# Performance work log

Hardware: AMD Instinct MI355X
Metric: run time of the kernel (lower is better)

## Reference

```python
import jax, jax.numpy as jnp
import numpy as np
import math

B, S, D = 4, 4096, 256

def _linear(x, W, b):
    return jnp.einsum('bsd,ed->bse', x, W) + b

def _attn(x, Wq, bq, Wk, bk, Wv, bv, d):
    Q = _linear(x, Wq, bq)
    K = _linear(x, Wk, bk)
    V = _linear(x, Wv, bv)
    scores = jnp.einsum('bqd,bkd->bqk', Q, K) / math.sqrt(d)  # [B,S,S]
    w = jax.nn.softmax(scores, axis=-1)
    return jnp.einsum('bqk,bkd->bqd', w, V)

def setup_inputs() -> dict:
    key = jax.random.key(0)
    ks = jax.random.split(key, 32)
    p = {}
    p['x'] = jax.random.normal(ks[0], (B, S, D), dtype=jnp.float32)
    p['eps'] = jax.random.normal(ks[1], (B, S, D), dtype=jnp.float32)
    i = 2
    for name in ['Wq1','Wk1','Wv1','Wq2','Wk2','Wv2','Wmu','Wlv']:
        p[name] = 0.02 * jax.random.normal(ks[i], (D, D), dtype=jnp.float32); i += 1
    for name in ['bq1','bk1','bv1','bq2','bk2','bv2','bmu','blv']:
        p[name] = jnp.zeros((D,), dtype=jnp.float32)
    p['Wg'] = 0.02 * jax.random.normal(ks[i], (1, D), dtype=jnp.float32); i += 1
    p['bg'] = jnp.zeros((1,), dtype=jnp.float32)
    p['gamma'] = jnp.ones((D,), dtype=jnp.float32)
    p['beta'] = jnp.zeros((D,), dtype=jnp.float32)
    return p

def reference(x, eps, Wq1, Wk1, Wv1, Wq2, Wk2, Wv2, Wmu, Wlv,
              bq1, bk1, bv1, bq2, bk2, bv2, bmu, blv, Wg, bg, gamma, beta):
    d = x.shape[-1]
    h1 = _attn(x, Wq1, bq1, Wk1, bk1, Wv1, bv1, d)
    h2 = _attn(h1, Wq2, bq2, Wk2, bk2, Wv2, bv2, d)
    mu = _linear(h2, Wmu, bmu)
    logvar = _linear(h2, Wlv, blv)
    std = jnp.exp(0.5 * logvar)
    z = jax.nn.elu(mu + eps * std)
    p_gate = jax.nn.sigmoid(_linear(h2.mean(axis=1)[:, None, :], Wg, bg))[:, 0, 0]  # [B]
    y = x + z
    mean = y.mean(axis=-1, keepdims=True)
    var = y.var(axis=-1, keepdims=True)
    out = (y - mean) / jnp.sqrt(var + 1e-5) * gamma + beta
    return (out, mu, logvar, p_gate)
```

## Files before the change

kernel.cpp:

```cpp
#include <hip/hip_runtime.h>
#include <hip/hip_bf16.h>
#include <hip/hip_fp8.h>
#include <cstdint>
#include <cstddef>


#define S_LEN 4096
#define DMODEL 256
#define NBATCH 4
#define MTOT (NBATCH * S_LEN)

typedef __bf16 bf16;
typedef __bf16 bf16x8 __attribute__((ext_vector_type(8)));
typedef float f32x4 __attribute__((ext_vector_type(4)));
typedef float f32x16 __attribute__((ext_vector_type(16)));
typedef unsigned char u8;
typedef unsigned int u32;

__device__ __forceinline__ f32x4 mfma16(bf16x8 a, bf16x8 b, f32x4 c) {
  return __builtin_amdgcn_mfma_f32_16x16x32_bf16(a, b, c, 0, 0, 0);
}
__device__ __forceinline__ f32x16 mfma32f8(long a, long b, f32x16 c) {
  return __builtin_amdgcn_mfma_f32_32x32x16_fp8_fp8(a, b, c, 0, 0, 0);
}

__device__ __forceinline__ void async16(const void* g, void* lds) {
  __builtin_amdgcn_global_load_lds(
      (const __attribute__((address_space(1))) unsigned int*)g,
      (__attribute__((address_space(3))) unsigned int*)lds, 16, 0, 0);
}

__device__ __forceinline__ unsigned short f2bfbits(float f) {
  return __builtin_bit_cast(unsigned short, (bf16)f);
}
__device__ __forceinline__ u8 f2fp8(float f) {
  __hip_fp8_e4m3 t(f);
  return *(u8*)&t;
}

struct WPtrs { const float* p[8]; };

__global__ void cast_all_kernel(const f32x4* __restrict__ x, WPtrs wp,
                                ushort4* __restrict__ x16, ushort4* __restrict__ w16) {
  int bx = blockIdx.x, t = threadIdx.x;
  const f32x4* src;
  ushort4* dst;
  if (bx < 4096) {
    src = x + (size_t)bx * 256 + t;
    dst = x16 + (size_t)bx * 256 + t;
  } else {
    int r = bx - 4096;
    int m = r >> 6;
    int i = (r & 63) * 256 + t;
    src = (const f32x4*)wp.p[m] + i;
    dst = w16 + (size_t)m * 16384 + i;
  }
  f32x4 v = *src;
  ushort4 o;
  o.x = f2bfbits(v[0]); o.y = f2bfbits(v[1]); o.z = f2bfbits(v[2]); o.w = f2bfbits(v[3]);
  *dst = o;
}

struct GemmIO {
  const float* bias[3];
  void* out[3];
};

__global__ __launch_bounds__(256, 3) void gemm_qkv_kernel(const bf16* __restrict__ A,
                                                          const bf16* __restrict__ Wb,
                                                          GemmIO io) {
  __shared__ bf16 ldsA[128 * 64];
  __shared__ bf16 ldsB[128 * 64];
  const int t = threadIdx.x;
  const int m0 = blockIdx.x * 128;
  const int n0 = blockIdx.y * 128;
  const bf16* W = Wb + (size_t)blockIdx.z * 65536;
  const int w = t >> 6, l = t & 63, lm = l & 15, q = l >> 4;
  const int wr = (w >> 1) * 64, wc = (w & 1) * 64;

  f32x4 acc[4][4] = {};
#pragma unroll 1
  for (int it = 0; it < 4; ++it) {
    const int k0 = it * 64;
#pragma unroll
    for (int c = 0; c < 4; ++c) {
      int i = c * 256 + t;
      int r = i >> 3, c8 = (i & 7) ^ (r & 7);
      async16(A + (size_t)(m0 + r) * 256 + k0 + c8 * 8, &ldsA[i * 8]);
    }
#pragma unroll
    for (int c = 0; c < 4; ++c) {
      int i = c * 256 + t;
      int r = i >> 3, c8 = (i & 7) ^ (r & 7);
      async16(W + (size_t)(n0 + r) * 256 + k0 + c8 * 8, &ldsB[i * 8]);
    }
    __syncthreads();
#pragma unroll
    for (int ks = 0; ks < 2; ++ks) {
      bf16x8 af[4], bfr[4];
#pragma unroll
      for (int i = 0; i < 4; ++i) {
        int ra = wr + i * 16 + lm;
        af[i] = *(const bf16x8*)&ldsA[ra * 64 + ((((ks << 2) + q) ^ (ra & 7)) << 3)];
        int rb = wc + i * 16 + lm;
        bfr[i] = *(const bf16x8*)&ldsB[rb * 64 + ((((ks << 2) + q) ^ (rb & 7)) << 3)];
      }
#pragma unroll
      for (int i = 0; i < 4; ++i)
#pragma unroll
        for (int jj = 0; jj < 4; ++jj) acc[i][jj] = mfma16(af[i], bfr[jj], acc[i][jj]);
    }
    __syncthreads();
  }
  const float* bias = io.bias[blockIdx.z];
  if (blockIdx.z == 2) {
    bf16* out = (bf16*)io.out[2];
#pragma unroll
    for (int jj = 0; jj < 4; ++jj) {
      int col = n0 + wc + jj * 16 + lm;
      float bv = bias[col];
#pragma unroll
      for (int i = 0; i < 4; ++i) {
        int row = m0 + wr + i * 16 + q * 4;
#pragma unroll
        for (int r = 0; r < 4; ++r)
          out[(size_t)(row + r) * 256 + col] = (bf16)(acc[i][jj][r] + bv);
      }
    }
  } else {
    u8* out = (u8*)io.out[blockIdx.z];
#pragma unroll
    for (int jj = 0; jj < 4; ++jj) {
      int col = n0 + wc + jj * 16 + lm;
      float bv = bias[col];
#pragma unroll
      for (int i = 0; i < 4; ++i) {
        int row = m0 + wr + i * 16 + q * 4;
#pragma unroll
        for (int r = 0; r < 4; ++r)
          out[(size_t)(row + r) * 256 + col] = f2fp8(acc[i][jj][r] + bv);
      }
    }
  }
}

__global__ __launch_bounds__(256, 3) void gemm_f_kernel(const bf16* __restrict__ A,
                                                        const bf16* __restrict__ Wb, GemmIO io) {
  __shared__ bf16 ldsA[128 * 64];
  __shared__ bf16 ldsB[128 * 64];
  const int t = threadIdx.x;
  const int m0 = blockIdx.x * 128;
  const int n0 = blockIdx.y * 128;
  const bf16* W = Wb + (size_t)blockIdx.z * 65536;
  const int w = t >> 6, l = t & 63, lm = l & 15, q = l >> 4;
  const int wr = (w >> 1) * 64, wc = (w & 1) * 64;

  f32x4 acc[4][4] = {};
#pragma unroll 1
  for (int it = 0; it < 4; ++it) {
    const int k0 = it * 64;
#pragma unroll
    for (int c = 0; c < 4; ++c) {
      int i = c * 256 + t;
      int r = i >> 3, c8 = (i & 7) ^ (r & 7);
      async16(A + (size_t)(m0 + r) * 256 + k0 + c8 * 8, &ldsA[i * 8]);
    }
#pragma unroll
    for (int c = 0; c < 4; ++c) {
      int i = c * 256 + t;
      int r = i >> 3, c8 = (i & 7) ^ (r & 7);
      async16(W + (size_t)(n0 + r) * 256 + k0 + c8 * 8, &ldsB[i * 8]);
    }
    __syncthreads();
#pragma unroll
    for (int ks = 0; ks < 2; ++ks) {
      bf16x8 af[4], bfr[4];
#pragma unroll
      for (int i = 0; i < 4; ++i) {
        int ra = wr + i * 16 + lm;
        af[i] = *(const bf16x8*)&ldsA[ra * 64 + ((((ks << 2) + q) ^ (ra & 7)) << 3)];
        int rb = wc + i * 16 + lm;
        bfr[i] = *(const bf16x8*)&ldsB[rb * 64 + ((((ks << 2) + q) ^ (rb & 7)) << 3)];
      }
#pragma unroll
      for (int i = 0; i < 4; ++i)
#pragma unroll
        for (int jj = 0; jj < 4; ++jj) acc[i][jj] = mfma16(af[i], bfr[jj], acc[i][jj]);
    }
    __syncthreads();
  }
  const float* bias = io.bias[blockIdx.z];
  float* out = (float*)io.out[blockIdx.z];
#pragma unroll
  for (int jj = 0; jj < 4; ++jj) {
    int col = n0 + wc + jj * 16 + lm;
    float bv = bias[col];
#pragma unroll
    for (int i = 0; i < 4; ++i) {
      int row = m0 + wr + i * 16 + q * 4;
#pragma unroll
      for (int r = 0; r < 4; ++r)
        out[(size_t)(row + r) * 256 + col] = acc[i][jj][r] + bv;
    }
  }
}

__global__ void transpose_kernel(const bf16* __restrict__ src, u8* __restrict__ dst) {
  __shared__ bf16 tile[64][72];
  int s0 = blockIdx.x * 64, d0 = blockIdx.y * 64;
  size_t boff = (size_t)blockIdx.z * S_LEN * 256;
  size_t boffT = (size_t)blockIdx.z * 256 * S_LEN;
  int t = threadIdx.x;
#pragma unroll
  for (int rep = 0; rep < 16; ++rep) {
    int lin = rep * 256 + t;
    int r = lin >> 6, c = lin & 63;
    tile[r][c] = src[boff + (size_t)(s0 + r) * 256 + d0 + c];
  }
  __syncthreads();
#pragma unroll
  for (int rep = 0; rep < 16; ++rep) {
    int lin = rep * 256 + t;
    int r = lin >> 6, c = lin & 63;
    dst[boffT + (size_t)(d0 + r) * S_LEN + s0 + c] = f2fp8((float)tile[c][r]);
  }
}

__global__ __launch_bounds__(1024, 4) void flash_kernel(const u8* __restrict__ Q,
                                                        const u8* __restrict__ K,
                                                        const u8* __restrict__ Vt,
                                                        bf16* __restrict__ O) {
  __shared__ __align__(16) u8 ldsK[256 * 256];
  __shared__ __align__(16) u8 ldsV[256 * 256];
  __shared__ __align__(16) u8 ldsP[2 * 32 * 264];
  __shared__ float lb[64];

  const int id = blockIdx.x;
  const int xcd = id & 7;
  const int b = xcd >> 1;
  const int qt = (id >> 3) + ((xcd & 1) << 5);

  const u8* Qb = Q + (size_t)b * S_LEN * 256;
  const u8* Kb = K + (size_t)b * S_LEN * 256;
  const u8* Vb = Vt + (size_t)b * 256 * S_LEN;
  bf16* Ob = O + (size_t)b * S_LEN * 256;

  const int t = threadIdx.x, w = t >> 6, lane = t & 63;
  const int m31 = lane & 31, kh = lane >> 5;
  const int qg = w & 1, sub = w >> 1;
  const float CL2 = 0.09016844005556021f;

  if (t < 64) lb[t] = 0.f;

  int sld[4], skg[4], svg[4];
#pragma unroll
  for (int it = 0; it < 4; ++it) {
    int c = it * 1024 + t;
    sld[it] = c * 16;
    int kr = c >> 4, g = (c & 15) ^ (kr & 15);
    skg[it] = kr * 256 + g * 16;
    svg[it] = kr * S_LEN + g * 16;
  }
  const int kn = sub * 32 + m31;
  const int kbase = kn * 256 + kh * 8, knx = kn & 15;
  const int vd = sub * 32 + m31;
  const int vbase = vd * 256 + kh * 8, vdx = vd & 15;
  u8* pstore = &ldsP[qg * 8448 + m31 * 264 + sub * 32 + 4 * kh];
  const u8* pread = &ldsP[qg * 8448 + m31 * 264 + kh * 8];

  long qf[16];
  {
    const u8* qrow = Qb + (size_t)(qt * 64 + qg * 32 + m31) * 256 + kh * 8;
#pragma unroll
    for (int ks = 0; ks < 16; ++ks) qf[ks] = *(const long*)(qrow + ks * 16);
  }

  f32x16 o_acc = {};
  float l_w = 0.f;

#pragma unroll
  for (int it = 0; it < 4; ++it) async16(Kb + skg[it], &ldsK[sld[it]]);

#pragma unroll 1
  for (int j = 0; j < 16; ++j) {
    __syncthreads();
    {
      const u8* vg = Vb + j * 256;
#pragma unroll
      for (int it = 0; it < 4; ++it) async16(vg + svg[it], &ldsV[sld[it]]);
    }
    f32x16 s = {};
#pragma unroll
    for (int ks = 0; ks < 16; ++ks) {
      long kf = *(const long*)(&ldsK[kbase + ((ks ^ knx) << 4)]);
      s = mfma32f8(kf, qf[ks], s);
    }
    float p[16];
#pragma unroll
    for (int r = 0; r < 16; ++r) {
      p[r] = __builtin_amdgcn_exp2f(s[r] * CL2);
      l_w += p[r];
    }
#pragma unroll
    for (int g = 0; g < 4; ++g) {
      u32 pk = (u32)f2fp8(p[4 * g]) | ((u32)f2fp8(p[4 * g + 1]) << 8) |
               ((u32)f2fp8(p[4 * g + 2]) << 16) | ((u32)f2fp8(p[4 * g + 3]) << 24);
      *(u32*)(pstore + g * 8) = pk;
    }
    __syncthreads();
    if (j + 1 < 16) {
      const u8* kg = Kb + (size_t)(j + 1) * 65536;
#pragma unroll
      for (int it = 0; it < 4; ++it) async16(kg + skg[it], &ldsK[sld[it]]);
    }
#pragma unroll
    for (int ks = 0; ks < 16; ++ks) {
      long pa = *(const long*)(pread + ks * 16);
      long vf = *(const long*)(&ldsV[vbase + ((ks ^ vdx) << 4)]);
      o_acc = mfma32f8(pa, vf, o_acc);
    }
  }

  l_w += __shfl_xor(l_w, 32, 64);
  if (kh == 0) atomicAdd(&lb[qg * 32 + m31], l_w);
  __syncthreads();

  bf16* orow = Ob + (size_t)(qt * 64 + qg * 32) * 256 + sub * 32;
#pragma unroll
  for (int reg = 0; reg < 16; ++reg) {
    const int row = (reg & 3) + 8 * (reg >> 2) + 4 * kh;
    orow[(size_t)row * 256 + m31] = (bf16)(o_acc[reg] / lb[qg * 32 + row]);
  }
}

__global__ __launch_bounds__(256) void gate_partial(const bf16* __restrict__ h,
                                                    float* __restrict__ part) {
  int bb = blockIdx.y;
  const bf16* hb = h + (size_t)bb * S_LEN * 256 + (size_t)blockIdx.x * 64 * 256;
  int t = threadIdx.x;
  float acc = 0.f;
#pragma unroll 4
  for (int s = 0; s < 64; ++s) acc += (float)hb[s * 256 + t];
  part[((size_t)bb * 64 + blockIdx.x) * 256 + t] = acc;
}

__global__ __launch_bounds__(256) void gate_final(const float* __restrict__ part,
                                                  const float* __restrict__ Wg,
                                                  const float* __restrict__ bg,
                                                  float* __restrict__ pg) {
  int bb = blockIdx.x, t = threadIdx.x;
  const float* p = part + (size_t)bb * 64 * 256;
  float acc = 0.f;
#pragma unroll 4
  for (int c = 0; c < 64; ++c) acc += p[c * 256 + t];
  acc *= Wg[t] * (1.0f / 4096.0f);
  __shared__ float red[256];
  red[t] = acc;
  __syncthreads();
  if (t < 64) {
    float a = red[t] + red[t + 64] + red[t + 128] + red[t + 192];
#pragma unroll
    for (int d = 1; d < 64; d <<= 1) a += __shfl_xor(a, d, 64);
    if (t == 0) pg[bb] = 1.0f / (1.0f + __expf(-(a + bg[0])));
  }
}

__global__ __launch_bounds__(256) void epilogue_kernel(const float* __restrict__ x,
                                                       const float* __restrict__ eps,
                                                       const float* __restrict__ mu,
                                                       const float* __restrict__ lv,
                                                       const float* __restrict__ gamma,
                                                       const float* __restrict__ beta,
                                                       float* __restrict__ out) {
  size_t base = (size_t)blockIdx.x * 1024 + (threadIdx.x >> 6) * 256;
  int l = threadIdx.x & 63;
  f32x4 xv = ((const f32x4*)(x + base))[l];
  f32x4 ev = ((const f32x4*)(eps + base))[l];
  f32x4 mv = ((const f32x4*)(mu + base))[l];
  f32x4 vv = ((const f32x4*)(lv + base))[l];
  f32x4 y;
  float s = 0.f, s2 = 0.f;
#pragma unroll
  for (int c = 0; c < 4; ++c) {
    float z = mv[c] + ev[c] * __expf(0.5f * vv[c]);
    z = z > 0.f ? z : (__expf(z) - 1.f);
    float yy = xv[c] + z;
    y[c] = yy;
    s += yy;
    s2 += yy * yy;
  }
#pragma unroll
  for (int d = 1; d < 64; d <<= 1) {
    s += __shfl_xor(s, d, 64);
    s2 += __shfl_xor(s2, d, 64);
  }
  float mean = s * (1.f / 256.f);
  float var = s2 * (1.f / 256.f) - mean * mean;
  float rstd = rsqrtf(var + 1e-5f);
  f32x4 gv = ((const f32x4*)gamma)[l];
  f32x4 bv = ((const f32x4*)beta)[l];
  f32x4 o;
#pragma unroll
  for (int c = 0; c < 4; ++c) o[c] = (y[c] - mean) * rstd * gv[c] + bv[c];
  ((f32x4*)(out + base))[l] = o;
}

extern "C" void kernel_launch(void* const* d_in, const int* in_sizes, int n_in, void* d_out,
                              int out_size, void* d_ws, size_t ws_size, hipStream_t stream) {
  const float* x = (const float*)d_in[0];
  const float* eps = (const float*)d_in[1];
  const float* Wg = (const float*)d_in[18];
  const float* bg = (const float*)d_in[19];
  const float* gamma = (const float*)d_in[20];
  const float* beta = (const float*)d_in[21];

  char* ws = (char*)d_ws;
  bf16* x16 = (bf16*)(ws);
  bf16* h16 = (bf16*)(ws + 8388608);
  bf16* v16 = (bf16*)(ws + 16777216);
  u8* q8 = (u8*)(ws + 25165824);
  u8* k8 = (u8*)(ws + 29360128);
  u8* vt8 = (u8*)(ws + 33554432);
  bf16* w16 = (bf16*)(ws + 37748736);
  float* gpart = (float*)(ws + 38797312);

  float* out = (float*)d_out;
  float* mu = out + 4194304;
  float* lv = out + 8388608;
  float* pg = out + 12582912;

  WPtrs wp;
  for (int i = 0; i < 8; ++i) wp.p[i] = (const float*)d_in[2 + i];
  cast_all_kernel<<<4608, 256, 0, stream>>>((const f32x4*)x, wp, (ushort4*)x16, (ushort4*)w16);

  GemmIO io1;
  io1.bias[0] = (const float*)d_in[10];
  io1.bias[1] = (const float*)d_in[11];
  io1.bias[2] = (const float*)d_in[12];
  io1.out[0] = q8; io1.out[1] = k8; io1.out[2] = v16;
  gemm_qkv_kernel<<<dim3(128, 2, 3), 256, 0, stream>>>(x16, w16, io1);
  transpose_kernel<<<dim3(64, 4, 4), 256, 0, stream>>>(v16, vt8);
  flash_kernel<<<256, 1024, 0, stream>>>(q8, k8, vt8, h16);

  GemmIO io2;
  io2.bias[0] = (const float*)d_in[13];
  io2.bias[1] = (const float*)d_in[14];
  io2.bias[2] = (const float*)d_in[15];
  io2.out[0] = q8; io2.out[1] = k8; io2.out[2] = v16;
  gemm_qkv_kernel<<<dim3(128, 2, 3), 256, 0, stream>>>(h16, w16 + 3 * 65536, io2);
  transpose_kernel<<<dim3(64, 4, 4), 256, 0, stream>>>(v16, vt8);
  flash_kernel<<<256, 1024, 0, stream>>>(q8, k8, vt8, h16);

  GemmIO io3;
  io3.bias[0] = (const float*)d_in[16];
  io3.bias[1] = (const float*)d_in[17];
  io3.bias[2] = nullptr;
  io3.out[0] = mu; io3.out[1] = lv; io3.out[2] = nullptr;
  gemm_f_kernel<<<dim3(128, 2, 2), 256, 0, stream>>>(h16, w16 + 6 * 65536, io3);

  gate_partial<<<dim3(64, 4), 256, 0, stream>>>(h16, gpart);
  gate_final<<<4, 256, 0, stream>>>(gpart, Wg, bg, pg);
  epilogue_kernel<<<4096, 256, 0, stream>>>(x, eps, mu, lv, gamma, beta, out);
}
```

Measured before the change: 332.9 us.

## Permute K and V columns so flash kernel reads LDS with 16-byte loads

```diff
diff --git a/kernel.cpp b/kernel.cpp
--- a/kernel.cpp
+++ b/kernel.cpp
@@ -14,6 +14,7 @@
 typedef __bf16 bf16x8 __attribute__((ext_vector_type(8)));
 typedef float f32x4 __attribute__((ext_vector_type(4)));
 typedef float f32x16 __attribute__((ext_vector_type(16)));
+typedef long longx2 __attribute__((ext_vector_type(2)));
 typedef unsigned char u8;
 typedef unsigned int u32;
 
@@ -36,6 +37,9 @@
 __device__ __forceinline__ u8 f2fp8(float f) {
   __hip_fp8_e4m3 t(f);
   return *(u8*)&t;
+}
+__device__ __forceinline__ int permc(int v) {
+  return (((v >> 3) & 1) << 7) + (((v >> 4) & 15) << 3) + (v & 7);
 }
 
 struct WPtrs { const float* p[8]; };
@@ -132,13 +136,14 @@
 #pragma unroll
     for (int jj = 0; jj < 4; ++jj) {
       int col = n0 + wc + jj * 16 + lm;
+      int scol = (blockIdx.z == 1) ? permc(col) : col;
       float bv = bias[col];
 #pragma unroll
       for (int i = 0; i < 4; ++i) {
         int row = m0 + wr + i * 16 + q * 4;
 #pragma unroll
         for (int r = 0; r < 4; ++r)
-          out[(size_t)(row + r) * 256 + col] = f2fp8(acc[i][jj][r] + bv);
+          out[(size_t)(row + r) * 256 + scol] = f2fp8(acc[i][jj][r] + bv);
       }
     }
   }
@@ -222,7 +227,9 @@
   for (int rep = 0; rep < 16; ++rep) {
     int lin = rep * 256 + t;
     int r = lin >> 6, c = lin & 63;
-    dst[boffT + (size_t)(d0 + r) * S_LEN + s0 + c] = f2fp8((float)tile[c][r]);
+    int sg = s0 + c;
+    int sp = (sg & ~255) + permc(sg & 255);
+    dst[boffT + (size_t)(d0 + r) * S_LEN + sp] = f2fp8((float)tile[c][r]);
   }
 }
 
@@ -232,7 +239,7 @@
                                                         bf16* __restrict__ O) {
   __shared__ __align__(16) u8 ldsK[256 * 256];
   __shared__ __align__(16) u8 ldsV[256 * 256];
-  __shared__ __align__(16) u8 ldsP[2 * 32 * 264];
+  __shared__ __align__(16) u8 ldsP[2 * 32 * 256];
   __shared__ float lb[64];
 
   const int id = blockIdx.x;
@@ -257,16 +264,19 @@
   for (int it = 0; it < 4; ++it) {
     int c = it * 1024 + t;
     sld[it] = c * 16;
-    int kr = c >> 4, g = (c & 15) ^ (kr & 15);
+    int kr = c >> 4, g = (c & 15) ^ (kr & 7);
     skg[it] = kr * 256 + g * 16;
     svg[it] = kr * S_LEN + g * 16;
   }
   const int kn = sub * 32 + m31;
-  const int kbase = kn * 256 + kh * 8, knx = kn & 15;
+  const u8* kbase = &ldsK[kn * 256 + kh * 128];
+  const int kx = kn & 7;
   const int vd = sub * 32 + m31;
-  const int vbase = vd * 256 + kh * 8, vdx = vd & 15;
-  u8* pstore = &ldsP[qg * 8448 + m31 * 264 + sub * 32 + 4 * kh];
-  const u8* pread = &ldsP[qg * 8448 + m31 * 264 + kh * 8];
+  const u8* vbase = &ldsV[vd * 256 + kh * 128];
+  const int vx = vd & 7;
+  const u8* pread = &ldsP[qg * 8192 + m31 * 256 + kh * 128];
+  const int px = m31 & 7;
+  u8* pstore = &ldsP[qg * 8192 + m31 * 256 + ((sub ^ px) << 4) + 4 * kh];
 
   long qf[16];
   {
@@ -291,9 +301,10 @@
     }
     f32x16 s = {};
 #pragma unroll
-    for (int ks = 0; ks < 16; ++ks) {
-      long kf = *(const long*)(&ldsK[kbase + ((ks ^ knx) << 4)]);
-      s = mfma32f8(kf, qf[ks], s);
+    for (int m = 0; m < 8; ++m) {
+      longx2 kf = *(const longx2*)(kbase + ((m ^ kx) << 4));
+      s = mfma32f8(kf.x, qf[2 * m], s);
+      s = mfma32f8(kf.y, qf[2 * m + 1], s);
     }
     float p[16];
 #pragma unroll
@@ -302,10 +313,10 @@
       l_w += p[r];
     }
 #pragma unroll
-    for (int g = 0; g < 4; ++g) {
-      u32 pk = (u32)f2fp8(p[4 * g]) | ((u32)f2fp8(p[4 * g + 1]) << 8) |
-               ((u32)f2fp8(p[4 * g + 2]) << 16) | ((u32)f2fp8(p[4 * g + 3]) << 24);
-      *(u32*)(pstore + g * 8) = pk;
+    for (int g2 = 0; g2 < 4; ++g2) {
+      int pk = __builtin_amdgcn_cvt_pk_fp8_f32(p[4 * g2], p[4 * g2 + 1], 0, false);
+      pk = __builtin_amdgcn_cvt_pk_fp8_f32(p[4 * g2 + 2], p[4 * g2 + 3], pk, true);
+      *(u32*)(pstore + (g2 & 1) * 128 + (g2 >> 1) * 8) = (u32)pk;
     }
     __syncthreads();
     if (j + 1 < 16) {
@@ -314,10 +325,11 @@
       for (int it = 0; it < 4; ++it) async16(kg + skg[it], &ldsK[sld[it]]);
     }
 #pragma unroll
-    for (int ks = 0; ks < 16; ++ks) {
-      long pa = *(const long*)(pread + ks * 16);
-      long vf = *(const long*)(&ldsV[vbase + ((ks ^ vdx) << 4)]);
-      o_acc = mfma32f8(pa, vf, o_acc);
+    for (int m = 0; m < 8; ++m) {
+      longx2 pa = *(const longx2*)(pread + ((m ^ px) << 4));
+      longx2 vf = *(const longx2*)(vbase + ((m ^ vx) << 4));
+      o_acc = mfma32f8(pa.x, vf.x, o_acc);
+      o_acc = mfma32f8(pa.y, vf.y, o_acc);
     }
   }
 
```

Result: faster. 321.9 us (-3.3%).
